# Kernel tuning notes

Hardware: AMD Instinct MI355X
Metric: run time of the kernel (lower is better)

The kernel has to match this reference:

```python
import jax, jax.numpy as jnp
import numpy as np

N_CODEBOOKS = 9
CODEBOOK_SIZE = 1024
CODEBOOK_DIM = 8
INPUT_DIM = 128
B, T = 16, 4096


def setup_inputs() -> dict:
    key = jax.random.key(0)
    ks = jax.random.split(key, 7)
    x = jax.random.normal(ks[0], (B, 2 * INPUT_DIM, T), dtype=jnp.float32)
    noise = jax.random.normal(ks[1], (B, INPUT_DIM, T), dtype=jnp.float32)
    # per-codebook params (stacked over the quantizer axis)
    in_w = jax.random.normal(ks[2], (N_CODEBOOKS, CODEBOOK_DIM, INPUT_DIM), dtype=jnp.float32) * 0.08
    in_b = jax.random.normal(ks[3], (N_CODEBOOKS, CODEBOOK_DIM), dtype=jnp.float32) * 0.01
    codebook = jax.random.normal(ks[4], (N_CODEBOOKS, CODEBOOK_SIZE, CODEBOOK_DIM), dtype=jnp.float32)
    out_w = jax.random.normal(ks[5], (N_CODEBOOKS, INPUT_DIM, CODEBOOK_DIM), dtype=jnp.float32) * 0.08
    out_b = jax.random.normal(ks[6], (N_CODEBOOKS, INPUT_DIM), dtype=jnp.float32) * 0.01
    return {"x": x, "noise": noise, "in_w": in_w, "in_b": in_b,
            "codebook": codebook, "out_w": out_w, "out_b": out_b}


def _l2norm(v, eps=1e-12):
    n = jnp.linalg.norm(v, axis=-1, keepdims=True)
    return v / jnp.maximum(n, eps)


def reference(x, noise, in_w, in_b, codebook, out_w, out_b):
    # --- vae_sample ---
    mean, scale = jnp.split(x, 2, axis=1)
    stdev = jax.nn.softplus(scale) + 1e-4
    var = stdev * stdev
    kl = jnp.mean(jnp.sum(mean * mean + var - jnp.log(var) - 1.0, axis=1))
    z = noise * stdev + mean  # [B, D, T]

    # --- ResidualVectorQuantize (eval mode, all codebooks) ---
    residual = z
    z_q = jnp.zeros_like(z)
    commitment_loss = jnp.float32(0.0)
    codebook_loss = jnp.float32(0.0)
    codes, lats = [], []
    b, _, t = z.shape
    for i in range(N_CODEBOOKS):
        # in_proj (1x1 conv)
        z_e = jnp.einsum("cd,bdt->bct", in_w[i], residual) + in_b[i][None, :, None]
        enc = z_e.transpose(0, 2, 1).reshape(b * t, CODEBOOK_DIM)
        enc_n = _l2norm(enc)
        cb_n = _l2norm(codebook[i])
        # squared L2 distance between normalized vectors
        dist = (jnp.sum(enc_n * enc_n, axis=1, keepdims=True)
                - 2.0 * enc_n @ cb_n.T
                + jnp.sum(cb_n * cb_n, axis=1)[None, :])
        idx = jnp.argmin(dist, axis=1).reshape(b, t)  # [B, T]
        zq_i = codebook[i][idx].transpose(0, 2, 1)  # [B, c, T] (raw codebook)
        # mse_loss(...).mean([1,2]).mean() == global mean
        commitment_loss = commitment_loss + jnp.mean((z_e - jax.lax.stop_gradient(zq_i)) ** 2)
        codebook_loss = codebook_loss + jnp.mean((zq_i - jax.lax.stop_gradient(z_e)) ** 2)
        # straight-through estimator
        zq_st = z_e + jax.lax.stop_gradient(zq_i - z_e)
        out = jnp.einsum("dc,bct->bdt", out_w[i], zq_st) + out_b[i][None, :, None]
        z_q = z_q + out
        residual = residual - out
        codes.append(idx)
        lats.append(z_e)
    codes = jnp.stack(codes, axis=1)          # [B, N, T]
    latents = jnp.concatenate(lats, axis=1)   # [B, N*c, T]
    commitment_loss = commitment_loss / N_CODEBOOKS
    codebook_loss = codebook_loss / N_CODEBOOKS
    return z_q, kl, commitment_loss, codebook_loss, codes, latents
```

## Files before the change

### kernel.cpp

```cpp
#include <hip/hip_runtime.h>
#include <cstdint>
#include <cstddef>

constexpr int T   = 4096;
constexpr int BB  = 16;
constexpr int D   = 128;
constexpr int CB  = 1024;
constexpr int CD  = 8;
constexpr int NCB = 9;

constexpr int TBLK = 64;
constexpr int NTHR = 512;
constexpr int NW   = 8;
constexpr int ZLS  = 66;

constexpr size_t OFF_ZQ    = 0;
constexpr size_t OFF_SCAL  = (size_t)BB * D * T;
constexpr size_t OFF_CODES = OFF_SCAL + 3;
constexpr size_t OFF_LAT   = OFF_CODES + (size_t)BB * NCB * T;

constexpr size_t AFR_U32 = (size_t)NCB * 64 * 2 * 64 * 4;
constexpr size_t H2C_F32 = (size_t)NCB * CB;
constexpr size_t AFW_U32 = (size_t)2 * 6 * 2 * 5 * 64 * 4;
constexpr size_t CM_F32  = (size_t)NCB * 72 * 8;
constexpr size_t OBS_F32 = 128;
constexpr size_t BEF_F32 = 72;
constexpr size_t OP_F32  = (size_t)NCB * CB * D;

typedef short bf16x8 __attribute__((ext_vector_type(8)));
typedef float f32x4  __attribute__((ext_vector_type(4)));

__device__ __forceinline__ unsigned short f2bf(float f) {
    unsigned u = __float_as_uint(f);
    return (unsigned short)((u + (((u >> 16) & 1u) + 0x7FFFu)) >> 16);
}
__device__ __forceinline__ float bf2f(unsigned short b) {
    return __uint_as_float((unsigned)b << 16);
}

constexpr int PAIR_A[6] = {0, 0, 1, 1, 2, 0};
constexpr int PAIR_B[6] = {0, 1, 0, 1, 0, 2};

__device__ __forceinline__ unsigned short splitterm(float xv, int term) {
    unsigned short t0 = f2bf(xv); if (term == 0) return t0;
    float r1 = xv - bf2f(t0);
    unsigned short t1 = f2bf(r1); if (term == 1) return t1;
    float r2 = r1 - bf2f(t1);
    return f2bf(r2);
}

__global__ void prep_kernel(const float* __restrict__ codebook,
                            const float* __restrict__ in_w,
                            const float* __restrict__ in_b,
                            const float* __restrict__ out_w,
                            const float* __restrict__ out_b,
                            unsigned* __restrict__ afr,
                            float* __restrict__ h2c,
                            unsigned* __restrict__ afw,
                            float* __restrict__ CMt,
                            float* __restrict__ obs,
                            float* __restrict__ bef,
                            float* __restrict__ OPt,
                            float* __restrict__ scal) {
    const int gid = blockIdx.x * blockDim.x + threadIdx.x;
    if (gid == 0) { scal[0] = 0.f; scal[1] = 0.f; scal[2] = 0.f; }

    if (gid < NCB * CB) {
        const int e  = gid;
        const int i  = e >> 10;
        const int en = e & 1023;
        const int et = en >> 4;
        const int m  = en & 15;

        float v[CD]; float s2 = 0.f;
#pragma unroll
        for (int j = 0; j < CD; ++j) { v[j] = codebook[(size_t)e * CD + j]; s2 = fmaf(v[j], v[j], s2); }
        float inv = 1.0f / fmaxf(sqrtf(s2), 1e-12f);
        float cn[CD]; float c2 = 0.f;
#pragma unroll
        for (int j = 0; j < CD; ++j) { cn[j] = v[j] * inv; c2 = fmaf(cn[j], cn[j], c2); }
        h2c[e] = -0.5f * c2;

        unsigned pk[3][4];
#pragma unroll
        for (int w = 0; w < 4; ++w) {
            float x0 = cn[2 * w], x1 = cn[2 * w + 1];
            unsigned short a0 = f2bf(x0); float r0 = x0 - bf2f(a0);
            unsigned short a1 = f2bf(r0); float q0 = r0 - bf2f(a1);
            unsigned short a2 = f2bf(q0);
            unsigned short b0 = f2bf(x1); float r1 = x1 - bf2f(b0);
            unsigned short b1 = f2bf(r1); float q1 = r1 - bf2f(b1);
            unsigned short b2 = f2bf(q1);
            pk[0][w] = (unsigned)a0 | ((unsigned)b0 << 16);
            pk[1][w] = (unsigned)a1 | ((unsigned)b1 << 16);
            pk[2][w] = (unsigned)a2 | ((unsigned)b2 << 16);
        }
        const int At[8] = {0, 1, 2, 0, 1, 0, 2, 1};
#pragma unroll
        for (int kh = 0; kh < 2; ++kh) {
#pragma unroll
            for (int h = 0; h < 4; ++h) {
                int A1 = At[kh * 4 + (h >> 1)];
                int A2 = At[kh * 4 + 2 + (h >> 1)];
                int dw = (h & 1) * 2;
                size_t off = ((((size_t)i * 64 + et) * 2 + kh) * 64 + (h * 16 + m)) * 4;
                afr[off + 0] = pk[A1][dw];
                afr[off + 1] = pk[A1][dw + 1];
                afr[off + 2] = pk[A2][dw];
                afr[off + 3] = pk[A2][dw + 1];
            }
        }
        return;
    }
    if (gid < 2 * NCB * CB) {
        const int e = gid - NCB * CB;
        const int i = e >> 10;
        float cv[CD];
#pragma unroll
        for (int d = 0; d < CD; ++d) cv[d] = codebook[(size_t)e * CD + d];
        const float* ow = out_w + (size_t)i * D * CD;
        float* dst = OPt + (size_t)e * D;
        for (int r = 0; r < D; ++r) {
            float a = 0.f;
#pragma unroll
            for (int d = 0; d < CD; ++d) a = fmaf(ow[r * CD + d], cv[d], a);
            dst[r] = a;
        }
        return;
    }
    if (gid < 2 * NCB * CB + NCB * 72) {
        const int idx = gid - 2 * NCB * CB;
        const int j = idx / 72, r = idx - j * 72;
        const float* wi = in_w + (size_t)r * D;
        const float* ow = out_w + (size_t)j * D * CD;
        float a[CD];
#pragma unroll
        for (int d = 0; d < CD; ++d) a[d] = 0.f;
        for (int k = 0; k < D; ++k) {
            float w = wi[k];
#pragma unroll
            for (int d = 0; d < CD; ++d) a[d] = fmaf(w, ow[k * CD + d], a[d]);
        }
#pragma unroll
        for (int d = 0; d < CD; ++d) CMt[((size_t)j * 72 + r) * CD + d] = a[d];
        return;
    }
    if (gid < 2 * NCB * CB + NCB * 72 + 128) {
        const int r = gid - (2 * NCB * CB + NCB * 72);
        float a = 0.f;
        for (int i = 0; i < NCB; ++i) a += out_b[(size_t)i * D + r];
        obs[r] = a;
        return;
    }
    if (gid < 2 * NCB * CB + NCB * 72 + 128 + 72) {
        const int row = gid - (2 * NCB * CB + NCB * 72 + 128);
        const int ic  = row >> 3;
        const float* wi = in_w + (size_t)row * D;
        float a = in_b[row];
        for (int j = 0; j < ic; ++j) {
            const float* ob = out_b + (size_t)j * D;
            float s = 0.f;
            for (int k = 0; k < D; ++k) s = fmaf(wi[k], ob[k], s);
            a -= s;
        }
        bef[row] = a;
        return;
    }
    if (gid < 2 * NCB * CB + NCB * 72 + 128 + 72 + 7680) {
        int idx = gid - (2 * NCB * CB + NCB * 72 + 128 + 72);
        const int lane = idx & 63; idx >>= 6;
        const int mt = idx % 5; idx /= 5;
        const int kq = idx & 1; idx >>= 1;
        const int p  = idx % 6;
        const int P  = idx / 6;
        const int h  = lane >> 4, m = lane & 15;
        const int row = mt * 16 + m;
        const int term = PAIR_A[p];
        const int D0 = P * 64 + kq * 32 + h * 4;
        const int doff[4][2] = {{0, 1}, {2, 3}, {16, 17}, {18, 19}};
        unsigned wv[4];
#pragma unroll
        for (int w = 0; w < 4; ++w) {
            unsigned short lo = 0, hi = 0;
            if (row < 72) {
                lo = splitterm(in_w[(size_t)row * D + D0 + doff[w][0]], term);
                hi = splitterm(in_w[(size_t)row * D + D0 + doff[w][1]], term);
            }
            wv[w] = (unsigned)lo | ((unsigned)hi << 16);
        }
        *reinterpret_cast<uint4*>(afw + ((size_t)(((P * 6 + p) * 2 + kq) * 5 + mt) * 64 + lane) * 4)
            = make_uint4(wv[0], wv[1], wv[2], wv[3]);
        return;
    }
}

__global__ __launch_bounds__(NTHR, 4)
void rvq_kernel(const float* __restrict__ x,
                const float* __restrict__ noise,
                const float* __restrict__ codebook,
                const unsigned* __restrict__ afr,
                const float* __restrict__ h2c,
                const unsigned* __restrict__ afw,
                const float* __restrict__ CMt,
                const float* __restrict__ obs,
                const float* __restrict__ bef,
                const float* __restrict__ OPt,
                float* __restrict__ o_zq,
                float* __restrict__ o_scal,
                float* __restrict__ o_codes,
                float* __restrict__ o_lat) {
    __shared__ char     zbuf[24576];
    __shared__ unsigned es[TBLK * 12];
    __shared__ float    redS[NW * TBLK];
    __shared__ int      redI[NW * TBLK];
    __shared__ int      cidx[NCB * TBLK];
    __shared__ float    redw[2 * NW];

    uint2* zs = reinterpret_cast<uint2*>(zbuf);
    float* Zl = reinterpret_cast<float*>(zbuf);

    const int tid = threadIdx.x;
    const int c   = tid & 63;
    const int s   = tid >> 6;
    const int su  = __builtin_amdgcn_readfirstlane(s);
    const int b   = blockIdx.x >> 6;
    const int t0  = (blockIdx.x & 63) << 6;
    const int t   = t0 + c;

    const int l  = tid & 63;
    const int h  = l >> 4;
    const int nl = l & 15;

    const int mtbase = (su < 4) ? 0 : 3;
    const int nmt    = (su < 4) ? 3 : 2;
    float kl_local = 0.f;
    f32x4 acc[3];
#pragma unroll
    for (int q = 0; q < 3; ++q) {
        int row0 = (mtbase + q) * 16 + h * 4;
        if (q < nmt && row0 < 72) acc[q] = *reinterpret_cast<const f32x4*>(bef + row0);
        else                      acc[q] = f32x4{0.f, 0.f, 0.f, 0.f};
    }

#pragma unroll 1
    for (int P = 0; P < 2; ++P) {
        {
            const int r0 = P * 64 + su * 8;
            const float* xm = x     + (size_t)b * 2 * D * T + (size_t)r0 * T + t;
            const float* xs = xm    + (size_t)D * T;
            const float* nz = noise + (size_t)b * D * T     + (size_t)r0 * T + t;
            float zrow[8];
#pragma unroll
            for (int k = 0; k < 8; ++k) {
                float m  = xm[(size_t)k * T];
                float sc = xs[(size_t)k * T];
                float nv = nz[(size_t)k * T];
                float sp  = fmaxf(sc, 0.f) + log1pf(expf(-fabsf(sc)));
                float sd  = sp + 1e-4f;
                float var = sd * sd;
                zrow[k]   = fmaf(nv, sd, m);
                kl_local += m * m + var - logf(var) - 1.0f;
            }
#pragma unroll
            for (int db = 0; db < 2; ++db) {
                unsigned w[3][2];
#pragma unroll
                for (int half = 0; half < 2; ++half) {
                    float x0 = zrow[db * 4 + half * 2], x1 = zrow[db * 4 + half * 2 + 1];
                    unsigned short a0 = f2bf(x0); float r1 = x0 - bf2f(a0);
                    unsigned short a1 = f2bf(r1); float r2 = r1 - bf2f(a1);
                    unsigned short a2 = f2bf(r2);
                    unsigned short b0 = f2bf(x1); float s1v = x1 - bf2f(b0);
                    unsigned short b1 = f2bf(s1v); float s2v = s1v - bf2f(b1);
                    unsigned short b2 = f2bf(s2v);
                    w[0][half] = (unsigned)a0 | ((unsigned)b0 << 16);
                    w[1][half] = (unsigned)a1 | ((unsigned)b1 << 16);
                    w[2][half] = (unsigned)a2 | ((unsigned)b2 << 16);
                }
#pragma unroll
                for (int tt = 0; tt < 3; ++tt)
                    zs[(tt * 16 + su * 2 + db) * 64 + c] = make_uint2(w[tt][0], w[tt][1]);
            }
        }
        __syncthreads();
        {
            const int colB = (su & 3) * 16 + nl;
#pragma unroll
            for (int p = 0; p < 6; ++p) {
#pragma unroll
                for (int kq = 0; kq < 2; ++kq) {
                    uint2 blo = zs[(PAIR_B[p] * 16 + kq * 8 + h) * 64 + colB];
                    uint2 bhi = zs[(PAIR_B[p] * 16 + kq * 8 + 4 + h) * 64 + colB];
                    uint4 bu = make_uint4(blo.x, blo.y, bhi.x, bhi.y);
                    bf16x8 bfr = *reinterpret_cast<bf16x8*>(&bu);
                    const uint4* Aw = reinterpret_cast<const uint4*>(afw)
                                      + (size_t)(((P * 6 + p) * 2 + kq) * 5) * 64 + l;
#pragma unroll
                    for (int q = 0; q < 3; ++q) {
                        if (q < nmt) {
                            uint4 au = Aw[(size_t)(mtbase + q) * 64];
                            bf16x8 af = *reinterpret_cast<bf16x8*>(&au);
                            acc[q] = __builtin_amdgcn_mfma_f32_16x16x32_bf16(af, bfr, acc[q], 0, 0, 0);
                        }
                    }
                }
            }
        }
        __syncthreads();
    }
#pragma unroll
    for (int q = 0; q < 3; ++q) {
        if (q < nmt) {
#pragma unroll
            for (int r = 0; r < 4; ++r)
                Zl[((mtbase + q) * 16 + h * 4 + r) * ZLS + (su & 3) * 16 + nl] = acc[q][r];
        }
    }

    float loss_local = 0.f;

    for (int i = 0; i < NCB; ++i) {
        __syncthreads();

        if (tid < 64) {
            float v[CD]; float n2 = 0.f;
#pragma unroll
            for (int j = 0; j < CD; ++j) { v[j] = Zl[(i * CD + j) * ZLS + tid]; n2 = fmaf(v[j], v[j], n2); }
            float inv = 1.0f / fmaxf(sqrtf(n2), 1e-12f);
            unsigned pk[3][4];
#pragma unroll
            for (int w = 0; w < 4; ++w) {
                float x0 = v[2 * w] * inv, x1 = v[2 * w + 1] * inv;
                unsigned short a0 = f2bf(x0); float r0 = x0 - bf2f(a0);
                unsigned short a1 = f2bf(r0); float q0 = r0 - bf2f(a1);
                unsigned short a2 = f2bf(q0);
                unsigned short b0 = f2bf(x1); float r1 = x1 - bf2f(b0);
                unsigned short b1 = f2bf(r1); float q1 = r1 - bf2f(b1);
                unsigned short b2 = f2bf(q1);
                pk[0][w] = (unsigned)a0 | ((unsigned)b0 << 16);
                pk[1][w] = (unsigned)a1 | ((unsigned)b1 << 16);
                pk[2][w] = (unsigned)a2 | ((unsigned)b2 << 16);
            }
            uint4* ep = reinterpret_cast<uint4*>(&es[(size_t)tid * 12]);
            ep[0] = make_uint4(pk[0][0], pk[0][1], pk[0][2], pk[0][3]);
            ep[1] = make_uint4(pk[1][0], pk[1][1], pk[1][2], pk[1][3]);
            ep[2] = make_uint4(pk[2][0], pk[2][1], pk[2][2], pk[2][3]);
        }
        {
            float la = Zl[(i * CD + su) * ZLS + c];
            o_lat[(size_t)b * (NCB * CD) * T + (size_t)(i * CD + su) * T + t] = la;
        }
        __syncthreads();

        bf16x8 bfrag[4][2];
        {
            const int dwo = (h & 1) * 2;
            const int tA  = h >> 1;
            const int tB  = 1 + (h >> 1);
#pragma unroll
            for (int pt = 0; pt < 4; ++pt) {
                const int col = pt * 16 + nl;
                uint2 lo0 = *reinterpret_cast<const uint2*>(&es[col * 12 + 0 * 4 + dwo]);
                uint2 hi0 = *reinterpret_cast<const uint2*>(&es[col * 12 + tA * 4 + dwo]);
                uint2 lh1 = *reinterpret_cast<const uint2*>(&es[col * 12 + tB * 4 + dwo]);
                uint4 t0v = make_uint4(lo0.x, lo0.y, hi0.x, hi0.y);
                uint4 t1v = make_uint4(lh1.x, lh1.y, lh1.x, lh1.y);
                bfrag[pt][0] = *reinterpret_cast<bf16x8*>(&t0v);
                bfrag[pt][1] = *reinterpret_cast<bf16x8*>(&t1v);
            }
        }

        float best[4] = {-3.0e38f, -3.0e38f, -3.0e38f, -3.0e38f};
        int   bidx[4] = {0, 0, 0, 0};
        {
            const uint4* Ab = reinterpret_cast<const uint4*>(afr)
                              + ((size_t)(i * 64 + su * 8) * 2) * 64 + l;
            const f32x4* Hb = reinterpret_cast<const f32x4*>(h2c)
                              + (size_t)i * 256 + su * 32;
            int eb = su * 128 + h * 4;
#pragma unroll 2
            for (int e8 = 0; e8 < 8; ++e8) {
                uint4 ua0 = Ab[0];
                uint4 ua1 = Ab[64];
                f32x4 hv  = Hb[e8 * 4 + h];
                bf16x8 a0 = *reinterpret_cast<bf16x8*>(&ua0);
                bf16x8 a1 = *reinterpret_cast<bf16x8*>(&ua1);
#pragma unroll
                for (int pt = 0; pt < 4; ++pt) {
                    f32x4 accd = __builtin_amdgcn_mfma_f32_16x16x32_bf16(a0, bfrag[pt][0], hv, 0, 0, 0);
                    accd = __builtin_amdgcn_mfma_f32_16x16x32_bf16(a1, bfrag[pt][1], accd, 0, 0, 0);
#pragma unroll
                    for (int r = 0; r < 4; ++r) {
                        float sc = accd[r];
                        if (sc > best[pt]) { best[pt] = sc; bidx[pt] = eb + r; }
                    }
                }
                Ab += 128; eb += 16;
            }
        }

#pragma unroll
        for (int off = 16; off <= 32; off <<= 1) {
#pragma unroll
            for (int pt = 0; pt < 4; ++pt) {
                float ob = __shfl_xor(best[pt], off, 64);
                int   oi = __shfl_xor(bidx[pt], off, 64);
                bool tk = (ob > best[pt]) || (ob == best[pt] && oi < bidx[pt]);
                if (tk) { best[pt] = ob; bidx[pt] = oi; }
            }
        }
        if (l < 16) {
#pragma unroll
            for (int pt = 0; pt < 4; ++pt) {
                redS[su * 64 + pt * 16 + l] = best[pt];
                redI[su * 64 + pt * 16 + l] = bidx[pt];
            }
        }
        __syncthreads();

        float bsc = redS[c];
        int   bi  = redI[c];
#pragma unroll
        for (int ww = 1; ww < NW; ++ww) {
            float v2 = redS[ww * TBLK + c];
            int   vi = redI[ww * TBLK + c];
            if (v2 > bsc) { bsc = v2; bi = vi; }
        }
        cidx[i * TBLK + c] = bi;
        if (s == 0) o_codes[(size_t)b * NCB * T + (size_t)i * T + t] = (float)bi;

        float cv[CD];
        {
            const float4* cr4 = (const float4*)(codebook + ((size_t)i * CB + bi) * CD);
            float4 qa = cr4[0], qb = cr4[1];
            cv[0] = qa.x; cv[1] = qa.y; cv[2] = qa.z; cv[3] = qa.w;
            cv[4] = qb.x; cv[5] = qb.y; cv[6] = qb.z; cv[7] = qb.w;
            if (s == 0) {
#pragma unroll
                for (int j = 0; j < CD; ++j) {
                    float dd = cv[j] - Zl[(i * CD + j) * ZLS + c];
                    loss_local = fmaf(dd, dd, loss_local);
                }
            }
        }

        {
            const int nf = 64 - 8 * i;
            for (int rr = su; rr < nf; rr += NW) {
                const int row = (i + 1) * 8 + rr;
                float zv = Zl[row * ZLS + c];
                const float* cm = CMt + ((size_t)i * 72 + row) * CD;
#pragma unroll
                for (int d2 = 0; d2 < CD; ++d2) zv = fmaf(-cm[d2], cv[d2], zv);
                Zl[row * ZLS + c] = zv;
            }
        }
    }
    __syncthreads();

    {
        f32x4 oa[4];
#pragma unroll
        for (int kb = 0; kb < 4; ++kb)
            oa[kb] = *reinterpret_cast<const f32x4*>(obs + su * 16 + kb * 4);
#pragma unroll
        for (int i2 = 0; i2 < NCB; ++i2) {
            int code = cidx[i2 * TBLK + c];
            const f32x4* op = reinterpret_cast<const f32x4*>(OPt + ((size_t)(i2 * CB + code)) * D + su * 16);
#pragma unroll
            for (int kb = 0; kb < 4; ++kb) oa[kb] += op[kb];
        }
        float* oq = o_zq + (size_t)b * D * T + (size_t)(su * 16) * T + t;
#pragma unroll
        for (int kb = 0; kb < 4; ++kb)
#pragma unroll
            for (int r = 0; r < 4; ++r)
                oq[(size_t)(kb * 4 + r) * T] = oa[kb][r];
    }

    float v = kl_local;
#pragma unroll
    for (int o = 32; o > 0; o >>= 1) v += __shfl_down(v, o, 64);
    float w2 = loss_local;
#pragma unroll
    for (int o = 32; o > 0; o >>= 1) w2 += __shfl_down(w2, o, 64);
    if ((tid & 63) == 0) { redw[s] = v; redw[NW + s] = w2; }
    __syncthreads();
    if (tid == 0) {
        float ks = 0.f, ls = 0.f;
#pragma unroll
        for (int q = 0; q < NW; ++q) { ks += redw[q]; ls += redw[NW + q]; }
        atomicAdd(&o_scal[0], ks * (1.0f / 65536.0f));
        float lsn = ls * (1.0f / (524288.0f * 9.0f));
        atomicAdd(&o_scal[1], lsn);
        atomicAdd(&o_scal[2], lsn);
    }
}

extern "C" void kernel_launch(void* const* d_in, const int* in_sizes, int n_in,
                              void* d_out, int out_size, void* d_ws, size_t ws_size,
                              hipStream_t stream) {
    const float* x        = (const float*)d_in[0];
    const float* noise    = (const float*)d_in[1];
    const float* in_w     = (const float*)d_in[2];
    const float* in_b     = (const float*)d_in[3];
    const float* codebook = (const float*)d_in[4];
    const float* out_w    = (const float*)d_in[5];
    const float* out_b    = (const float*)d_in[6];

    float* out     = (float*)d_out;
    float* o_zq    = out + OFF_ZQ;
    float* o_scal  = out + OFF_SCAL;
    float* o_codes = out + OFF_CODES;
    float* o_lat   = out + OFF_LAT;

    unsigned* afr = (unsigned*)d_ws;
    float*    h2c = (float*)(afr + AFR_U32);
    unsigned* afw = (unsigned*)(h2c + H2C_F32);
    float*    CMt = (float*)(afw + AFW_U32);
    float*    obs = CMt + CM_F32;
    float*    bef = obs + OBS_F32;
    float*    OPt = bef + BEF_F32;

    const int prep_total = 2 * NCB * CB + NCB * 72 + 128 + 72 + 7680;
    prep_kernel<<<(prep_total + 255) / 256, 256, 0, stream>>>(
        codebook, in_w, in_b, out_w, out_b, afr, h2c, afw, CMt, obs, bef, OPt, o_scal);

    dim3 grid(BB * (T / TBLK));
    rvq_kernel<<<grid, NTHR, 0, stream>>>(x, noise, codebook,
                                          afr, h2c, afw, CMt, obs, bef, OPt,
                                          o_zq, o_scal, o_codes, o_lat);
}
```

Before: 385.9 us.

## Process two 64-column time tiles per block to reuse codebook fragments

```diff
diff --git a/kernel.cpp b/kernel.cpp
--- a/kernel.cpp
+++ b/kernel.cpp
@@ -209,23 +209,24 @@
                 float* __restrict__ o_scal,
                 float* __restrict__ o_codes,
                 float* __restrict__ o_lat) {
-    __shared__ char     zbuf[24576];
-    __shared__ unsigned es[TBLK * 12];
-    __shared__ float    redS[NW * TBLK];
-    __shared__ int      redI[NW * TBLK];
-    __shared__ int      cidx[NCB * TBLK];
-    __shared__ float    redw[2 * NW];
-
-    uint2* zs = reinterpret_cast<uint2*>(zbuf);
-    float* Zl = reinterpret_cast<float*>(zbuf);
+    __shared__ char sbuf[24576 + 2 * 19008];
+
+    uint2*    zs   = reinterpret_cast<uint2*>(sbuf);
+    unsigned* esA  = reinterpret_cast<unsigned*>(sbuf);
+    unsigned* esB  = reinterpret_cast<unsigned*>(sbuf + 3072);
+    float*    redS = reinterpret_cast<float*>(sbuf + 6144);
+    int*      redI = reinterpret_cast<int*>(sbuf + 10240);
+    int*      cidx = reinterpret_cast<int*>(sbuf + 14336);
+    float*    redw = reinterpret_cast<float*>(sbuf + 18944);
+    float*    ZlA  = reinterpret_cast<float*>(sbuf + 24576);
+    float*    ZlB  = reinterpret_cast<float*>(sbuf + 24576 + 19008);
 
     const int tid = threadIdx.x;
     const int c   = tid & 63;
     const int s   = tid >> 6;
     const int su  = __builtin_amdgcn_readfirstlane(s);
-    const int b   = blockIdx.x >> 6;
-    const int t0  = (blockIdx.x & 63) << 6;
-    const int t   = t0 + c;
+    const int b   = blockIdx.x >> 5;
+    const int t0  = (blockIdx.x & 31) << 7;
 
     const int l  = tid & 63;
     const int h  = l >> 4;
@@ -234,98 +235,112 @@
     const int mtbase = (su < 4) ? 0 : 3;
     const int nmt    = (su < 4) ? 3 : 2;
     float kl_local = 0.f;
-    f32x4 acc[3];
-#pragma unroll
-    for (int q = 0; q < 3; ++q) {
-        int row0 = (mtbase + q) * 16 + h * 4;
-        if (q < nmt && row0 < 72) acc[q] = *reinterpret_cast<const f32x4*>(bef + row0);
-        else                      acc[q] = f32x4{0.f, 0.f, 0.f, 0.f};
-    }
 
 #pragma unroll 1
-    for (int P = 0; P < 2; ++P) {
-        {
-            const int r0 = P * 64 + su * 8;
-            const float* xm = x     + (size_t)b * 2 * D * T + (size_t)r0 * T + t;
-            const float* xs = xm    + (size_t)D * T;
-            const float* nz = noise + (size_t)b * D * T     + (size_t)r0 * T + t;
-            float zrow[8];
-#pragma unroll
-            for (int k = 0; k < 8; ++k) {
-                float m  = xm[(size_t)k * T];
-                float sc = xs[(size_t)k * T];
-                float nv = nz[(size_t)k * T];
-                float sp  = fmaxf(sc, 0.f) + log1pf(expf(-fabsf(sc)));
-                float sd  = sp + 1e-4f;
-                float var = sd * sd;
-                zrow[k]   = fmaf(nv, sd, m);
-                kl_local += m * m + var - logf(var) - 1.0f;
-            }
-#pragma unroll
-            for (int db = 0; db < 2; ++db) {
-                unsigned w[3][2];
-#pragma unroll
-                for (int half = 0; half < 2; ++half) {
-                    float x0 = zrow[db * 4 + half * 2], x1 = zrow[db * 4 + half * 2 + 1];
-                    unsigned short a0 = f2bf(x0); float r1 = x0 - bf2f(a0);
-                    unsigned short a1 = f2bf(r1); float r2 = r1 - bf2f(a1);
-                    unsigned short a2 = f2bf(r2);
-                    unsigned short b0 = f2bf(x1); float s1v = x1 - bf2f(b0);
-                    unsigned short b1 = f2bf(s1v); float s2v = s1v - bf2f(b1);
-                    unsigned short b2 = f2bf(s2v);
-                    w[0][half] = (unsigned)a0 | ((unsigned)b0 << 16);
-                    w[1][half] = (unsigned)a1 | ((unsigned)b1 << 16);
-                    w[2][half] = (unsigned)a2 | ((unsigned)b2 << 16);
-                }
-#pragma unroll
-                for (int tt = 0; tt < 3; ++tt)
-                    zs[(tt * 16 + su * 2 + db) * 64 + c] = make_uint2(w[tt][0], w[tt][1]);
-            }
-        }
-        __syncthreads();
-        {
-            const int colB = (su & 3) * 16 + nl;
-#pragma unroll
-            for (int p = 0; p < 6; ++p) {
-#pragma unroll
-                for (int kq = 0; kq < 2; ++kq) {
-                    uint2 blo = zs[(PAIR_B[p] * 16 + kq * 8 + h) * 64 + colB];
-                    uint2 bhi = zs[(PAIR_B[p] * 16 + kq * 8 + 4 + h) * 64 + colB];
-                    uint4 bu = make_uint4(blo.x, blo.y, bhi.x, bhi.y);
-                    bf16x8 bfr = *reinterpret_cast<bf16x8*>(&bu);
-                    const uint4* Aw = reinterpret_cast<const uint4*>(afw)
-                                      + (size_t)(((P * 6 + p) * 2 + kq) * 5) * 64 + l;
-#pragma unroll
-                    for (int q = 0; q < 3; ++q) {
-                        if (q < nmt) {
-                            uint4 au = Aw[(size_t)(mtbase + q) * 64];
-                            bf16x8 af = *reinterpret_cast<bf16x8*>(&au);
-                            acc[q] = __builtin_amdgcn_mfma_f32_16x16x32_bf16(af, bfr, acc[q], 0, 0, 0);
+    for (int tl = 0; tl < 2; ++tl) {
+        float* Zl = tl ? ZlB : ZlA;
+        const int t = t0 + tl * 64 + c;
+        f32x4 acc[3];
+#pragma unroll
+        for (int q = 0; q < 3; ++q) {
+            int row0 = (mtbase + q) * 16 + h * 4;
+            if (q < nmt && row0 < 72) acc[q] = *reinterpret_cast<const f32x4*>(bef + row0);
+            else                      acc[q] = f32x4{0.f, 0.f, 0.f, 0.f};
+        }
+
+#pragma unroll 1
+        for (int P = 0; P < 2; ++P) {
+            {
+                const int r0 = P * 64 + su * 8;
+                const float* xm = x     + (size_t)b * 2 * D * T + (size_t)r0 * T + t;
+                const float* xs = xm    + (size_t)D * T;
+                const float* nz = noise + (size_t)b * D * T     + (size_t)r0 * T + t;
+                float zrow[8];
+#pragma unroll
+                for (int k = 0; k < 8; ++k) {
+                    float m  = xm[(size_t)k * T];
+                    float sc = xs[(size_t)k * T];
+                    float nv = nz[(size_t)k * T];
+                    float sp  = fmaxf(sc, 0.f) + log1pf(expf(-fabsf(sc)));
+                    float sd  = sp + 1e-4f;
+                    float var = sd * sd;
+                    zrow[k]   = fmaf(nv, sd, m);
+                    kl_local += m * m + var - logf(var) - 1.0f;
+                }
+#pragma unroll
+                for (int db = 0; db < 2; ++db) {
+                    unsigned w[3][2];
+#pragma unroll
+                    for (int half = 0; half < 2; ++half) {
+                        float x0 = zrow[db * 4 + half * 2], x1 = zrow[db * 4 + half * 2 + 1];
+                        unsigned short a0 = f2bf(x0); float r1 = x0 - bf2f(a0);
+                        unsigned short a1 = f2bf(r1); float r2 = r1 - bf2f(a1);
+                        unsigned short a2 = f2bf(r2);
+                        unsigned short b0 = f2bf(x1); float s1v = x1 - bf2f(b0);
+                        unsigned short b1 = f2bf(s1v); float s2v = s1v - bf2f(b1);
+                        unsigned short b2 = f2bf(s2v);
+                        w[0][half] = (unsigned)a0 | ((unsigned)b0 << 16);
+                        w[1][half] = (unsigned)a1 | ((unsigned)b1 << 16);
+                        w[2][half] = (unsigned)a2 | ((unsigned)b2 << 16);
+                    }
+#pragma unroll
+                    for (int tt = 0; tt < 3; ++tt)
+                        zs[(tt * 16 + su * 2 + db) * 64 + c] = make_uint2(w[tt][0], w[tt][1]);
+                }
+            }
+            __syncthreads();
+            {
+                const int colB = (su & 3) * 16 + nl;
+#pragma unroll
+                for (int p = 0; p < 6; ++p) {
+#pragma unroll
+                    for (int kq = 0; kq < 2; ++kq) {
+                        uint2 blo = zs[(PAIR_B[p] * 16 + kq * 8 + h) * 64 + colB];
+                        uint2 bhi = zs[(PAIR_B[p] * 16 + kq * 8 + 4 + h) * 64 + colB];
+                        uint4 bu = make_uint4(blo.x, blo.y, bhi.x, bhi.y);
+                        bf16x8 bfr = *reinterpret_cast<bf16x8*>(&bu);
+                        const uint4* Aw = reinterpret_cast<const uint4*>(afw)
+                                          + (size_t)(((P * 6 + p) * 2 + kq) * 5) * 64 + l;
+#pragma unroll
+                        for (int q = 0; q < 3; ++q) {
+                            if (q < nmt) {
+                                uint4 au = Aw[(size_t)(mtbase + q) * 64];
+                                bf16x8 af = *reinterpret_cast<bf16x8*>(&au);
+                                acc[q] = __builtin_amdgcn_mfma_f32_16x16x32_bf16(af, bfr, acc[q], 0, 0, 0);
+                            }
                         }
                     }
                 }
             }
-        }
-        __syncthreads();
-    }
-#pragma unroll
-    for (int q = 0; q < 3; ++q) {
-        if (q < nmt) {
-#pragma unroll
-            for (int r = 0; r < 4; ++r)
-                Zl[((mtbase + q) * 16 + h * 4 + r) * ZLS + (su & 3) * 16 + nl] = acc[q][r];
+            __syncthreads();
+        }
+#pragma unroll
+        for (int q = 0; q < 3; ++q) {
+            if (q < nmt) {
+                const int row0 = (mtbase + q) * 16 + h * 4;
+                if (row0 < 72) {
+#pragma unroll
+                    for (int r = 0; r < 4; ++r)
+                        Zl[(row0 + r) * ZLS + (su & 3) * 16 + nl] = acc[q][r];
+                }
+            }
         }
     }
 
     float loss_local = 0.f;
+    const int tg = su >> 2;
+    const int sv = su & 3;
 
     for (int i = 0; i < NCB; ++i) {
         __syncthreads();
 
-        if (tid < 64) {
+        if (tid < 128) {
+            float*    Zl = (tid & 64) ? ZlB : ZlA;
+            unsigned* es = (tid & 64) ? esB : esA;
+            const int cc = tid & 63;
             float v[CD]; float n2 = 0.f;
 #pragma unroll
-            for (int j = 0; j < CD; ++j) { v[j] = Zl[(i * CD + j) * ZLS + tid]; n2 = fmaf(v[j], v[j], n2); }
+            for (int j = 0; j < CD; ++j) { v[j] = Zl[(i * CD + j) * ZLS + cc]; n2 = fmaf(v[j], v[j], n2); }
             float inv = 1.0f / fmaxf(sqrtf(n2), 1e-12f);
             unsigned pk[3][4];
 #pragma unroll
@@ -341,18 +356,20 @@
                 pk[1][w] = (unsigned)a1 | ((unsigned)b1 << 16);
                 pk[2][w] = (unsigned)a2 | ((unsigned)b2 << 16);
             }
-            uint4* ep = reinterpret_cast<uint4*>(&es[(size_t)tid * 12]);
+            uint4* ep = reinterpret_cast<uint4*>(&es[(size_t)cc * 12]);
             ep[0] = make_uint4(pk[0][0], pk[0][1], pk[0][2], pk[0][3]);
             ep[1] = make_uint4(pk[1][0], pk[1][1], pk[1][2], pk[1][3]);
             ep[2] = make_uint4(pk[2][0], pk[2][1], pk[2][2], pk[2][3]);
         }
         {
-            float la = Zl[(i * CD + su) * ZLS + c];
-            o_lat[(size_t)b * (NCB * CD) * T + (size_t)(i * CD + su) * T + t] = la;
+            float la0 = ZlA[(i * CD + su) * ZLS + c];
+            float la1 = ZlB[(i * CD + su) * ZLS + c];
+            o_lat[(size_t)b * (NCB * CD) * T + (size_t)(i * CD + su) * T + t0 + c]      = la0;
+            o_lat[(size_t)b * (NCB * CD) * T + (size_t)(i * CD + su) * T + t0 + 64 + c] = la1;
         }
         __syncthreads();
 
-        bf16x8 bfrag[4][2];
+        bf16x8 bfA[4][2], bfB[4][2];
         {
             const int dwo = (h & 1) * 2;
             const int tA  = h >> 1;
@@ -360,18 +377,31 @@
 #pragma unroll
             for (int pt = 0; pt < 4; ++pt) {
                 const int col = pt * 16 + nl;
-                uint2 lo0 = *reinterpret_cast<const uint2*>(&es[col * 12 + 0 * 4 + dwo]);
-                uint2 hi0 = *reinterpret_cast<const uint2*>(&es[col * 12 + tA * 4 + dwo]);
-                uint2 lh1 = *reinterpret_cast<const uint2*>(&es[col * 12 + tB * 4 + dwo]);
-                uint4 t0v = make_uint4(lo0.x, lo0.y, hi0.x, hi0.y);
-                uint4 t1v = make_uint4(lh1.x, lh1.y, lh1.x, lh1.y);
-                bfrag[pt][0] = *reinterpret_cast<bf16x8*>(&t0v);
-                bfrag[pt][1] = *reinterpret_cast<bf16x8*>(&t1v);
-            }
-        }
-
-        float best[4] = {-3.0e38f, -3.0e38f, -3.0e38f, -3.0e38f};
-        int   bidx[4] = {0, 0, 0, 0};
+                {
+                    uint2 lo0 = *reinterpret_cast<const uint2*>(&esA[col * 12 + 0 * 4 + dwo]);
+                    uint2 hi0 = *reinterpret_cast<const uint2*>(&esA[col * 12 + tA * 4 + dwo]);
+                    uint2 lh1 = *reinterpret_cast<const uint2*>(&esA[col * 12 + tB * 4 + dwo]);
+                    uint4 t0v = make_uint4(lo0.x, lo0.y, hi0.x, hi0.y);
+                    uint4 t1v = make_uint4(lh1.x, lh1.y, lh1.x, lh1.y);
+                    bfA[pt][0] = *reinterpret_cast<bf16x8*>(&t0v);
+                    bfA[pt][1] = *reinterpret_cast<bf16x8*>(&t1v);
+                }
+                {
+                    uint2 lo0 = *reinterpret_cast<const uint2*>(&esB[col * 12 + 0 * 4 + dwo]);
+                    uint2 hi0 = *reinterpret_cast<const uint2*>(&esB[col * 12 + tA * 4 + dwo]);
+                    uint2 lh1 = *reinterpret_cast<const uint2*>(&esB[col * 12 + tB * 4 + dwo]);
+                    uint4 t0v = make_uint4(lo0.x, lo0.y, hi0.x, hi0.y);
+                    uint4 t1v = make_uint4(lh1.x, lh1.y, lh1.x, lh1.y);
+                    bfB[pt][0] = *reinterpret_cast<bf16x8*>(&t0v);
+                    bfB[pt][1] = *reinterpret_cast<bf16x8*>(&t1v);
+                }
+            }
+        }
+
+        float bestA[4] = {-3.0e38f, -3.0e38f, -3.0e38f, -3.0e38f};
+        float bestB[4] = {-3.0e38f, -3.0e38f, -3.0e38f, -3.0e38f};
+        int   bidxA[4] = {0, 0, 0, 0};
+        int   bidxB[4] = {0, 0, 0, 0};
         {
             const uint4* Ab = reinterpret_cast<const uint4*>(afr)
                               + ((size_t)(i * 64 + su * 8) * 2) * 64 + l;
@@ -387,12 +417,16 @@
                 bf16x8 a1 = *reinterpret_cast<bf16x8*>(&ua1);
 #pragma unroll
                 for (int pt = 0; pt < 4; ++pt) {
-                    f32x4 accd = __builtin_amdgcn_mfma_f32_16x16x32_bf16(a0, bfrag[pt][0], hv, 0, 0, 0);
-                    accd = __builtin_amdgcn_mfma_f32_16x16x32_bf16(a1, bfrag[pt][1], accd, 0, 0, 0);
+                    f32x4 acA = __builtin_amdgcn_mfma_f32_16x16x32_bf16(a0, bfA[pt][0], hv, 0, 0, 0);
+                    acA = __builtin_amdgcn_mfma_f32_16x16x32_bf16(a1, bfA[pt][1], acA, 0, 0, 0);
+                    f32x4 acB = __builtin_amdgcn_mfma_f32_16x16x32_bf16(a0, bfB[pt][0], hv, 0, 0, 0);
+                    acB = __builtin_amdgcn_mfma_f32_16x16x32_bf16(a1, bfB[pt][1], acB, 0, 0, 0);
 #pragma unroll
                     for (int r = 0; r < 4; ++r) {
-                        float sc = accd[r];
-                        if (sc > best[pt]) { best[pt] = sc; bidx[pt] = eb + r; }
+                        float sa = acA[r];
+                        if (sa > bestA[pt]) { bestA[pt] = sa; bidxA[pt] = eb + r; }
+                        float sb = acB[r];
+                        if (sb > bestB[pt]) { bestB[pt] = sb; bidxB[pt] = eb + r; }
                     }
                 }
                 Ab += 128; eb += 16;
@@ -403,31 +437,42 @@
         for (int off = 16; off <= 32; off <<= 1) {
 #pragma unroll
             for (int pt = 0; pt < 4; ++pt) {
-                float ob = __shfl_xor(best[pt], off, 64);
-                int   oi = __shfl_xor(bidx[pt], off, 64);
-                bool tk = (ob > best[pt]) || (ob == best[pt] && oi < bidx[pt]);
-                if (tk) { best[pt] = ob; bidx[pt] = oi; }
+                float oa2 = __shfl_xor(bestA[pt], off, 64);
+                int   oi  = __shfl_xor(bidxA[pt], off, 64);
+                bool tk = (oa2 > bestA[pt]) || (oa2 == bestA[pt] && oi < bidxA[pt]);
+                if (tk) { bestA[pt] = oa2; bidxA[pt] = oi; }
+                float ob2 = __shfl_xor(bestB[pt], off, 64);
+                int   oj  = __shfl_xor(bidxB[pt], off, 64);
+                bool tk2 = (ob2 > bestB[pt]) || (ob2 == bestB[pt] && oj < bidxB[pt]);
+                if (tk2) { bestB[pt] = ob2; bidxB[pt] = oj; }
             }
         }
         if (l < 16) {
 #pragma unroll
             for (int pt = 0; pt < 4; ++pt) {
-                redS[su * 64 + pt * 16 + l] = best[pt];
-                redI[su * 64 + pt * 16 + l] = bidx[pt];
+                redS[(0 * 8 + su) * 64 + pt * 16 + l] = bestA[pt];
+                redI[(0 * 8 + su) * 64 + pt * 16 + l] = bidxA[pt];
+            }
+        } else if (l < 32) {
+#pragma unroll
+            for (int pt = 0; pt < 4; ++pt) {
+                redS[(1 * 8 + su) * 64 + pt * 16 + (l - 16)] = bestB[pt];
+                redI[(1 * 8 + su) * 64 + pt * 16 + (l - 16)] = bidxB[pt];
             }
         }
         __syncthreads();
 
-        float bsc = redS[c];
-        int   bi  = redI[c];
+        float bsc = redS[(tg * 8) * 64 + c];
+        int   bi  = redI[(tg * 8) * 64 + c];
 #pragma unroll
         for (int ww = 1; ww < NW; ++ww) {
-            float v2 = redS[ww * TBLK + c];
-            int   vi = redI[ww * TBLK + c];
+            float v2 = redS[(tg * 8 + ww) * 64 + c];
+            int   vi = redI[(tg * 8 + ww) * 64 + c];
             if (v2 > bsc) { bsc = v2; bi = vi; }
         }
-        cidx[i * TBLK + c] = bi;
-        if (s == 0) o_codes[(size_t)b * NCB * T + (size_t)i * T + t] = (float)bi;
+        cidx[(tg * NCB + i) * 64 + c] = bi;
+        if (su == 0) o_codes[(size_t)b * NCB * T + (size_t)i * T + t0 + c]      = (float)bi;
+        if (su == 4) o_codes[(size_t)b * NCB * T + (size_t)i * T + t0 + 64 + c] = (float)bi;
 
         float cv[CD];
         {
@@ -435,7 +480,8 @@
             float4 qa = cr4[0], qb = cr4[1];
             cv[0] = qa.x; cv[1] = qa.y; cv[2] = qa.z; cv[3] = qa.w;
             cv[4] = qb.x; cv[5] = qb.y; cv[6] = qb.z; cv[7] = qb.w;
-            if (s == 0) {
+            if (su == 0 || su == 4) {
+                float* Zl = tg ? ZlB : ZlA;
 #pragma unroll
                 for (int j = 0; j < CD; ++j) {
                     float dd = cv[j] - Zl[(i * CD + j) * ZLS + c];
@@ -445,8 +491,9 @@
         }
 
         {
+            float* Zl = tg ? ZlB : ZlA;
             const int nf = 64 - 8 * i;
-            for (int rr = su; rr < nf; rr += NW) {
+            for (int rr = sv; rr < nf; rr += 4) {
                 const int row = (i + 1) * 8 + rr;
                 float zv = Zl[row * ZLS + c];
                 const float* cm = CMt + ((size_t)i * 72 + row) * CD;
@@ -459,20 +506,20 @@
     __syncthreads();
 
     {
-        f32x4 oa[4];
-#pragma unroll
-        for (int kb = 0; kb < 4; ++kb)
-            oa[kb] = *reinterpret_cast<const f32x4*>(obs + su * 16 + kb * 4);
+        f32x4 oa[8];
+#pragma unroll
+        for (int kb = 0; kb < 8; ++kb)
+            oa[kb] = *reinterpret_cast<const f32x4*>(obs + sv * 32 + kb * 4);
 #pragma unroll
         for (int i2 = 0; i2 < NCB; ++i2) {
-            int code = cidx[i2 * TBLK + c];
-            const f32x4* op = reinterpret_cast<const f32x4*>(OPt + ((size_t)(i2 * CB + code)) * D + su * 16);
-#pragma unroll
-            for (int kb = 0; kb < 4; ++kb) oa[kb] += op[kb];
-        }
-        float* oq = o_zq + (size_t)b * D * T + (size_t)(su * 16) * T + t;
-#pragma unroll
-        for (int kb = 0; kb < 4; ++kb)
+            int code = cidx[(tg * NCB + i2) * 64 + c];
+            const f32x4* op = reinterpret_cast<const f32x4*>(OPt + ((size_t)(i2 * CB + code)) * D + sv * 32);
+#pragma unroll
+            for (int kb = 0; kb < 8; ++kb) oa[kb] += op[kb];
+        }
+        float* oq = o_zq + (size_t)b * D * T + (size_t)(sv * 32) * T + t0 + tg * 64 + c;
+#pragma unroll
+        for (int kb = 0; kb < 8; ++kb)
 #pragma unroll
             for (int r = 0; r < 4; ++r)
                 oq[(size_t)(kb * 4 + r) * T] = oa[kb][r];
@@ -526,7 +573,7 @@
     prep_kernel<<<(prep_total + 255) / 256, 256, 0, stream>>>(
         codebook, in_w, in_b, out_w, out_b, afr, h2c, afw, CMt, obs, bef, OPt, o_scal);
 
-    dim3 grid(BB * (T / TBLK));
+    dim3 grid(BB * (T / (TBLK * 2)));
     rvq_kernel<<<grid, NTHR, 0, stream>>>(x, noise, codebook,
                                           afr, h2c, afw, CMt, obs, bef, OPt,
                                           o_zq, o_scal, o_codes, o_lat);
```

New measurement: 363.3 us. -5.9%, faster.
